# Kernel optimization log

Measured on AMD Instinct MI355X. Metric: run time of the kernel, lower is better.

The kernel has to match this reference:

```python
import jax, jax.numpy as jnp
import numpy as np
import math

B, S, D, H = 4, 1024, 1024, 16
F = 4 * D
DK = D // H

def layer_norm(x, g, b, eps=1e-5):
    mu = jnp.mean(x, axis=-1, keepdims=True)
    var = jnp.var(x, axis=-1, keepdims=True)
    return (x - mu) * jax.lax.rsqrt(var + eps) * g + b

def setup_inputs() -> dict:
    key = jax.random.key(0)
    ks = jax.random.split(key, 8)
    s = 0.02
    return {
        "x": jax.random.normal(ks[0], (B, S, D), dtype=jnp.float32),
        "Wq": jax.random.normal(ks[1], (D, D), dtype=jnp.float32) * s,
        "Wk": jax.random.normal(ks[2], (D, D), dtype=jnp.float32) * s,
        "Wv": jax.random.normal(ks[3], (D, D), dtype=jnp.float32) * s,
        "Wo": jax.random.normal(ks[4], (D, D), dtype=jnp.float32) * s,
        "w1": jax.random.normal(ks[5], (F, D), dtype=jnp.float32) * s,
        "b1": jnp.zeros((F,), dtype=jnp.float32),
        "w2": jax.random.normal(ks[6], (D, F), dtype=jnp.float32) * s,
        "b2": jnp.zeros((D,), dtype=jnp.float32),
        "ln1_g": jnp.ones((D,), dtype=jnp.float32),
        "ln1_b": jnp.zeros((D,), dtype=jnp.float32),
        "ln2_g": jnp.ones((D,), dtype=jnp.float32),
        "ln2_b": jnp.zeros((D,), dtype=jnp.float32),
        "mask": jnp.ones((B, S, S), dtype=jnp.int32),
    }

def reference(x, Wq, Wk, Wv, Wo, w1, b1, w2, b2, ln1_g, ln1_b, ln2_g, ln2_b, mask):
    # --- attention sublayer (pre-norm residual) ---
    h = layer_norm(x, ln1_g, ln1_b)
    def split_heads(t):  # [B,S,D] -> [B,H,S,DK]
        return t.reshape(B, S, H, DK).transpose(0, 2, 1, 3)
    q = split_heads(h @ Wq.T)
    k = split_heads(h @ Wk.T)
    v = split_heads(h @ Wv.T)
    scores = jnp.einsum('bhqd,bhkd->bhqk', q, k) / math.sqrt(DK)
    m = (mask[:, None, :, :] != 0)  # [B,1,S,S] broadcast over heads
    scores = jnp.where(m, scores, -1e9)
    p = jax.nn.softmax(scores, axis=-1)
    p = jnp.where(m, p, 0.0)
    ctx = jnp.einsum('bhqk,bhkd->bhqd', p, v)
    ctx = ctx.transpose(0, 2, 1, 3).reshape(B, S, D)
    x = x + ctx @ Wo.T
    # --- FFN sublayer (pre-norm residual) ---
    h2 = layer_norm(x, ln2_g, ln2_b)
    y = jax.nn.gelu(h2 @ w1.T + b1, approximate=False) @ w2.T + b2
    row_valid = jnp.sum(mask, axis=-1) > 0  # [B,S]
    y = jnp.where(row_valid[..., None], y, 0.0)
    return x + y
```

## Files before the change

kernel.cpp:

```cpp
#include <hip/hip_runtime.h>

typedef unsigned short u16;
typedef unsigned int   u32;
typedef unsigned long long u64;

typedef __bf16 bf16_t;
typedef bf16_t bf16x8 __attribute__((ext_vector_type(8)));
typedef float  f32x4  __attribute__((ext_vector_type(4)));

static constexpr int Bz = 4, Sq = 1024, Dm = 1024, Hn = 16, Ff = 4096, Mtok = 4096;
static constexpr int QS = 3072;

static __device__ __forceinline__ u16 f2bf(float f) {
  u32 u = __builtin_bit_cast(u32, f);
  u32 r = u + 0x7fff + ((u >> 16) & 1);
  return (u16)(r >> 16);
}

static __device__ __forceinline__ void gld16(const u16* g, u16* l) {
  __builtin_amdgcn_global_load_lds((const __attribute__((address_space(1))) u32*)g,
                                   (__attribute__((address_space(3))) u32*)l, 16, 0, 0);
}

__global__ void k_cvt(const float* __restrict__ src, u16* __restrict__ dst, int n4) {
  int i = blockIdx.x * 256 + threadIdx.x;
  if (i >= n4) return;
  float4 v = reinterpret_cast<const float4*>(src)[i];
  ushort4 o;
  o.x = f2bf(v.x); o.y = f2bf(v.y); o.z = f2bf(v.z); o.w = f2bf(v.w);
  reinterpret_cast<ushort4*>(dst)[i] = o;
}

__global__ void k_maskpack(const int* __restrict__ mask, u32* __restrict__ mb,
                           u32* __restrict__ rv) {
  int row = blockIdx.x;
  int t = threadIdx.x, w = t >> 6, lane = t & 63;
  const int* mrow = mask + (size_t)row * Sq;
  __shared__ u32 red[4];
  u32 any = 0;
#pragma unroll
  for (int i = 0; i < 4; i++) {
    int chunk = w * 4 + i;
    int k = chunk * 64 + lane;
    u64 bal = __ballot(mrow[k] != 0);
    any |= (u32)(bal | (bal >> 32));
    if (lane == 0) mb[(size_t)row * 32 + chunk * 2]     = (u32)bal;
    if (lane == 1) mb[(size_t)row * 32 + chunk * 2 + 1] = (u32)(bal >> 32);
  }
  if (lane == 0) red[w] = any;
  __syncthreads();
  if (t == 0) rv[row] = (red[0] | red[1] | red[2] | red[3]) ? 1u : 0u;
}

__global__ void k_ln(const float* __restrict__ x, const float* __restrict__ g,
                     const float* __restrict__ bb, u16* __restrict__ out) {
  int row = blockIdx.x, t = threadIdx.x;
  float4 v = reinterpret_cast<const float4*>(x + (size_t)row * Dm)[t];
  float s  = v.x + v.y + v.z + v.w;
  float s2 = v.x * v.x + v.y * v.y + v.z * v.z + v.w * v.w;
#pragma unroll
  for (int m = 1; m < 64; m <<= 1) { s += __shfl_xor(s, m); s2 += __shfl_xor(s2, m); }
  __shared__ float rs[4], rs2[4];
  int w = t >> 6;
  if ((t & 63) == 0) { rs[w] = s; rs2[w] = s2; }
  __syncthreads();
  s  = rs[0] + rs[1] + rs[2] + rs[3];
  s2 = rs2[0] + rs2[1] + rs2[2] + rs2[3];
  float mu  = s * (1.0f / Dm);
  float var = s2 * (1.0f / Dm) - mu * mu;
  float r = rsqrtf(var + 1e-5f);
  float4 gv = reinterpret_cast<const float4*>(g)[t];
  float4 bv = reinterpret_cast<const float4*>(bb)[t];
  ushort4 o;
  o.x = f2bf((v.x - mu) * r * gv.x + bv.x);
  o.y = f2bf((v.y - mu) * r * gv.y + bv.y);
  o.z = f2bf((v.z - mu) * r * gv.z + bv.z);
  o.w = f2bf((v.w - mu) * r * gv.w + bv.w);
  reinterpret_cast<ushort4*>(out + (size_t)row * Dm)[t] = o;
}

template <int MODE>
__global__ __launch_bounds__(256)
void k_gemm(const u16* __restrict__ A, const u16* __restrict__ Bw,
            int M, int N, int K,
            const float* __restrict__ bias, void* __restrict__ Cout) {
  __shared__ u16 As[128 * 64];
  __shared__ u16 Bs[128 * 64];
  const int t = threadIdx.x;
  const int lane = t & 63, w = t >> 6;
  const int wr = w >> 1, wc = w & 1;
  const int m0 = blockIdx.y * 128, n0 = blockIdx.x * 128;
  const int lr = lane & 15, lk = (lane >> 4) * 8;

  f32x4 acc[4][4] = {};

  for (int kt = 0; kt < K; kt += 64) {
#pragma unroll
    for (int i = 0; i < 4; i++) {
      int cc = i * 256 + t; int row = cc >> 3, c8 = cc & 7;
      gld16(A + (size_t)(m0 + row) * K + kt + c8 * 8, &As[cc * 8]);
    }
#pragma unroll
    for (int i = 0; i < 4; i++) {
      int cc = i * 256 + t; int row = cc >> 3, c8 = cc & 7;
      gld16(Bw + (size_t)(n0 + row) * K + kt + c8 * 8, &Bs[cc * 8]);
    }
    __syncthreads();
#pragma unroll
    for (int kk = 0; kk < 2; kk++) {
      bf16x8 af[4], bfg[4];
#pragma unroll
      for (int m = 0; m < 4; m++)
        af[m] = *reinterpret_cast<const bf16x8*>(&As[(wr * 64 + m * 16 + lr) * 64 + kk * 32 + lk]);
#pragma unroll
      for (int n = 0; n < 4; n++)
        bfg[n] = *reinterpret_cast<const bf16x8*>(&Bs[(wc * 64 + n * 16 + lr) * 64 + kk * 32 + lk]);
#pragma unroll
      for (int m = 0; m < 4; m++)
#pragma unroll
        for (int n = 0; n < 4; n++)
          acc[m][n] = __builtin_amdgcn_mfma_f32_16x16x32_bf16(af[m], bfg[n], acc[m][n], 0, 0, 0);
    }
    __syncthreads();
  }

#pragma unroll
  for (int m = 0; m < 4; m++) {
    const int rowb = m0 + wr * 64 + m * 16 + (lane >> 4) * 4;
#pragma unroll
    for (int n = 0; n < 4; n++) {
      const int col = n0 + wc * 64 + n * 16 + lr;
#pragma unroll
      for (int r = 0; r < 4; r++) {
        const int row = rowb + r;
        float v = acc[m][n][r];
        size_t idx = (size_t)row * N + col;
        if constexpr (MODE == 0) {
          ((u16*)Cout)[idx] = f2bf(v);
        } else {
          float xx = v + bias[col];
          float gl = 0.5f * xx * (1.0f + erff(xx * 0.70710678118f));
          ((u16*)Cout)[idx] = f2bf(gl);
        }
      }
    }
  }
}

template <int MODE>
__global__ __launch_bounds__(256)
void k_gemm64(const u16* __restrict__ A, const u16* __restrict__ Bw,
              int M, int N, int K,
              const float* __restrict__ resid, const float* __restrict__ bias,
              const u32* __restrict__ rv, float* __restrict__ Cout) {
  __shared__ u16 As[128 * 64];
  __shared__ u16 Bs[64 * 64];
  const int t = threadIdx.x;
  const int lane = t & 63, w = t >> 6;
  const int m0 = blockIdx.y * 128, n0 = blockIdx.x * 64;
  const int lr = lane & 15, lk = (lane >> 4) * 8;

  f32x4 acc[2][4] = {};

  for (int kt = 0; kt < K; kt += 64) {
#pragma unroll
    for (int i = 0; i < 4; i++) {
      int cc = i * 256 + t; int row = cc >> 3, c8 = cc & 7;
      gld16(A + (size_t)(m0 + row) * K + kt + c8 * 8, &As[cc * 8]);
    }
#pragma unroll
    for (int i = 0; i < 2; i++) {
      int cc = i * 256 + t; int row = cc >> 3, c8 = cc & 7;
      gld16(Bw + (size_t)(n0 + row) * K + kt + c8 * 8, &Bs[cc * 8]);
    }
    __syncthreads();
#pragma unroll
    for (int kk = 0; kk < 2; kk++) {
      bf16x8 af[2], bfg[4];
#pragma unroll
      for (int m = 0; m < 2; m++)
        af[m] = *reinterpret_cast<const bf16x8*>(&As[(w * 32 + m * 16 + lr) * 64 + kk * 32 + lk]);
#pragma unroll
      for (int n = 0; n < 4; n++)
        bfg[n] = *reinterpret_cast<const bf16x8*>(&Bs[(n * 16 + lr) * 64 + kk * 32 + lk]);
#pragma unroll
      for (int m = 0; m < 2; m++)
#pragma unroll
        for (int n = 0; n < 4; n++)
          acc[m][n] = __builtin_amdgcn_mfma_f32_16x16x32_bf16(af[m], bfg[n], acc[m][n], 0, 0, 0);
    }
    __syncthreads();
  }

#pragma unroll
  for (int m = 0; m < 2; m++) {
    const int rowb = m0 + w * 32 + m * 16 + (lane >> 4) * 4;
#pragma unroll
    for (int n = 0; n < 4; n++) {
      const int col = n0 + n * 16 + lr;
#pragma unroll
      for (int r = 0; r < 4; r++) {
        const int row = rowb + r;
        float v = acc[m][n][r];
        size_t idx = (size_t)row * N + col;
        if constexpr (MODE == 1) {
          Cout[idx] = resid[idx] + v;
        } else {
          float y = rv[row] ? (v + bias[col]) : 0.0f;
          Cout[idx] = resid[idx] + y;
        }
      }
    }
  }
}

__global__ __launch_bounds__(256)
void k_attn(const u16* __restrict__ qkv, const u32* __restrict__ mb,
            u16* __restrict__ ctxb) {
  __shared__ u16 Qs[64 * 64];
  __shared__ u16 Ks[64 * 64];
  __shared__ u16 Vts[64 * 64];
  __shared__ u16 Ps[4 * 16 * 64];
  const int t = threadIdx.x, lane = t & 63, w = t >> 6;
  const int q0 = blockIdx.x * 64;
  const int bh = blockIdx.y, b = bh >> 4, h = bh & 15;
  const int lr = lane & 15, lkq = (lane >> 4) * 8;
  const size_t baseq = (size_t)(b * Sq) * QS + h * 64;

  {
    int r = t >> 2, c0 = (t & 3) * 16;
    const u16* gp = qkv + baseq + (size_t)(q0 + r) * QS + c0;
    uint4 v0 = *reinterpret_cast<const uint4*>(gp);
    uint4 v1 = *reinterpret_cast<const uint4*>(gp + 8);
    int sw = (r & 7) << 3;
    *reinterpret_cast<uint4*>(&Qs[r * 64 + (c0 ^ sw)]) = v0;
    *reinterpret_cast<uint4*>(&Qs[r * 64 + ((c0 + 8) ^ sw)]) = v1;
  }
  __syncthreads();

  bf16x8 qf[2];
  const int qrow = w * 16 + lr;
#pragma unroll
  for (int kk = 0; kk < 2; kk++)
    qf[kk] = *reinterpret_cast<const bf16x8*>(&Qs[qrow * 64 + ((kk * 32 + lkq) ^ ((qrow & 7) << 3))]);

  float m_i[4] = {-1e30f, -1e30f, -1e30f, -1e30f};
  float l_i[4] = {0.f, 0.f, 0.f, 0.f};
  f32x4 accO[4] = {};
  const int rq0 = (lane >> 4) * 4;

  for (int kt = 0; kt < Sq / 64; kt++) {
    __syncthreads();
    {
      int r = t >> 2, c0 = (t & 3) * 16;
      const u16* gp = qkv + baseq + 1024 + (size_t)(kt * 64 + r) * QS + c0;
      uint4 v0 = *reinterpret_cast<const uint4*>(gp);
      uint4 v1 = *reinterpret_cast<const uint4*>(gp + 8);
      int sw = (r & 7) << 3;
      *reinterpret_cast<uint4*>(&Ks[r * 64 + (c0 ^ sw)]) = v0;
      *reinterpret_cast<uint4*>(&Ks[r * 64 + ((c0 + 8) ^ sw)]) = v1;
      const u16* gv = qkv + baseq + 2048 + (size_t)(kt * 64 + r) * QS + c0;
      u16 tmp[16];
      *reinterpret_cast<uint4*>(&tmp[0]) = *reinterpret_cast<const uint4*>(gv);
      *reinterpret_cast<uint4*>(&tmp[8]) = *reinterpret_cast<const uint4*>(gv + 8);
#pragma unroll
      for (int j = 0; j < 16; j++) {
        int d = c0 + j;
        Vts[d * 64 + (r ^ ((d & 7) << 3))] = tmp[j];
      }
    }
    __syncthreads();

    f32x4 sc[4];
#pragma unroll
    for (int n = 0; n < 4; n++) sc[n] = (f32x4){0.f, 0.f, 0.f, 0.f};
#pragma unroll
    for (int kk = 0; kk < 2; kk++) {
#pragma unroll
      for (int n = 0; n < 4; n++) {
        int krow = n * 16 + lr;
        bf16x8 kf = *reinterpret_cast<const bf16x8*>(
            &Ks[krow * 64 + ((kk * 32 + lkq) ^ ((krow & 7) << 3))]);
        sc[n] = __builtin_amdgcn_mfma_f32_16x16x32_bf16(qf[kk], kf, sc[n], 0, 0, 0);
      }
    }
    u32 mw[4][2];
#pragma unroll
    for (int r = 0; r < 4; r++) {
      int q = q0 + w * 16 + rq0 + r;
      mw[r][0] = mb[(size_t)(b * Sq + q) * 32 + kt * 2];
      mw[r][1] = mb[(size_t)(b * Sq + q) * 32 + kt * 2 + 1];
    }
    float rmax[4] = {-1e30f, -1e30f, -1e30f, -1e30f};
#pragma unroll
    for (int n = 0; n < 4; n++) {
      int kin = n * 16 + lr;
#pragma unroll
      for (int r = 0; r < 4; r++) {
        float sval = sc[n][r] * 0.125f;
        if (!((mw[r][kin >> 5] >> (kin & 31)) & 1)) sval = -1e9f;
        sc[n][r] = sval;
        rmax[r] = fmaxf(rmax[r], sval);
      }
    }
#pragma unroll
    for (int r = 0; r < 4; r++) {
#pragma unroll
      for (int mm = 1; mm < 16; mm <<= 1) rmax[r] = fmaxf(rmax[r], __shfl_xor(rmax[r], mm));
      float mnew = fmaxf(m_i[r], rmax[r]);
      float scale = __expf(m_i[r] - mnew);
      m_i[r] = mnew;
      l_i[r] *= scale;
#pragma unroll
      for (int n = 0; n < 4; n++) accO[n][r] *= scale;
    }
    float rsum[4] = {0.f, 0.f, 0.f, 0.f};
#pragma unroll
    for (int n = 0; n < 4; n++)
#pragma unroll
      for (int r = 0; r < 4; r++) {
        float p = __expf(sc[n][r] - m_i[r]);
        sc[n][r] = p;
        rsum[r] += p;
      }
#pragma unroll
    for (int r = 0; r < 4; r++) {
#pragma unroll
      for (int mm = 1; mm < 16; mm <<= 1) rsum[r] += __shfl_xor(rsum[r], mm);
      l_i[r] += rsum[r];
    }
#pragma unroll
    for (int n = 0; n < 4; n++)
#pragma unroll
      for (int r = 0; r < 4; r++) {
        int row = rq0 + r;
        Ps[w * 1024 + row * 64 + ((n * 16 + lr) ^ ((row & 7) << 3))] = f2bf(sc[n][r]);
      }
    asm volatile("s_waitcnt lgkmcnt(0)" ::: "memory");
    __builtin_amdgcn_sched_barrier(0);
    bf16x8 pf[2];
#pragma unroll
    for (int kk = 0; kk < 2; kk++)
      pf[kk] = *reinterpret_cast<const bf16x8*>(
          &Ps[w * 1024 + lr * 64 + ((kk * 32 + lkq) ^ ((lr & 7) << 3))]);
#pragma unroll
    for (int kk = 0; kk < 2; kk++) {
#pragma unroll
      for (int n = 0; n < 4; n++) {
        int d = n * 16 + lr;
        bf16x8 vf = *reinterpret_cast<const bf16x8*>(
            &Vts[d * 64 + ((kk * 32 + lkq) ^ ((d & 7) << 3))]);
        accO[n] = __builtin_amdgcn_mfma_f32_16x16x32_bf16(pf[kk], vf, accO[n], 0, 0, 0);
      }
    }
  }

#pragma unroll
  for (int r = 0; r < 4; r++) {
    float recip = (m_i[r] <= -0.9e9f || l_i[r] == 0.f) ? 0.f : 1.f / l_i[r];
    int grow = q0 + w * 16 + rq0 + r;
#pragma unroll
    for (int n = 0; n < 4; n++)
      ctxb[(size_t)(b * Sq + grow) * Dm + h * 64 + n * 16 + lr] = f2bf(accO[n][r] * recip);
  }
}

extern "C" void kernel_launch(void* const* d_in, const int* in_sizes, int n_in,
                              void* d_out, int out_size, void* d_ws, size_t ws_size,
                              hipStream_t stream) {
  const float* x     = (const float*)d_in[0];
  const float* Wq    = (const float*)d_in[1];
  const float* Wk    = (const float*)d_in[2];
  const float* Wv    = (const float*)d_in[3];
  const float* Wo    = (const float*)d_in[4];
  const float* w1    = (const float*)d_in[5];
  const float* b1    = (const float*)d_in[6];
  const float* w2    = (const float*)d_in[7];
  const float* b2    = (const float*)d_in[8];
  const float* ln1g  = (const float*)d_in[9];
  const float* ln1b  = (const float*)d_in[10];
  const float* ln2g  = (const float*)d_in[11];
  const float* ln2b  = (const float*)d_in[12];
  const int*   mask  = (const int*)d_in[13];
  float* out = (float*)d_out;

  char* ws = (char*)d_ws;
  const size_t MB = 1024 * 1024;
  u16* wqkv_b = (u16*)(ws + 0 * MB);
  u16* wo_b   = (u16*)(ws + 13 * MB / 2);
  u16* w1_b   = (u16*)(ws + 17 * MB / 2);
  u16* w2_b   = (u16*)(ws + 17 * MB);
  u16* h_b    = (u16*)(ws + 51 * MB / 2);
  u32* mbits  = (u32*)(ws + 34 * MB);
  u32* rv     = (u32*)(ws + 34 * MB + 600 * 1024);
  u16* qkv    = (u16*)(ws + 35 * MB);
  u16* ctxb   = (u16*)(ws + 121 * MB / 2);
  u16* a1b    = (u16*)(ws + 35 * MB);
  float* x1   = out;

  k_cvt<<<1024, 256, 0, stream>>>(Wq, wqkv_b,               262144);
  k_cvt<<<1024, 256, 0, stream>>>(Wk, wqkv_b + 1024 * 1024, 262144);
  k_cvt<<<1024, 256, 0, stream>>>(Wv, wqkv_b + 2048 * 1024, 262144);
  k_cvt<<<1024, 256, 0, stream>>>(Wo, wo_b, 262144);
  k_cvt<<<4096, 256, 0, stream>>>(w1, w1_b, 1048576);
  k_cvt<<<4096, 256, 0, stream>>>(w2, w2_b, 1048576);
  k_maskpack<<<4096, 256, 0, stream>>>(mask, mbits, rv);
  k_ln<<<4096, 256, 0, stream>>>(x, ln1g, ln1b, h_b);

  dim3 gqkv(QS / 128, Mtok / 128);
  k_gemm<0><<<gqkv, 256, 0, stream>>>(h_b, wqkv_b, Mtok, QS, Dm, nullptr, qkv);

  dim3 ga(Sq / 64, Bz * Hn);
  k_attn<<<ga, 256, 0, stream>>>(qkv, mbits, ctxb);

  dim3 gwo(Dm / 64, Mtok / 128);
  k_gemm64<1><<<gwo, 256, 0, stream>>>(ctxb, wo_b, Mtok, Dm, Dm, x, nullptr, nullptr, x1);

  k_ln<<<4096, 256, 0, stream>>>(x1, ln2g, ln2b, h_b);

  dim3 g2(Ff / 128, Mtok / 128);
  k_gemm<2><<<g2, 256, 0, stream>>>(h_b, w1_b, Mtok, Ff, Dm, b1, a1b);

  dim3 gw2(Dm / 64, Mtok / 128);
  k_gemm64<3><<<gw2, 256, 0, stream>>>(a1b, w2_b, Mtok, Dm, Ff, x1, b2, rv, out);
}
```

Measured before the change: 456.4 us.

## Emit transposed V from QKV GEMM and double-buffer K/V loads in attention

The QKV GEMM now writes the V slice directly in a per-head transposed layout, so attention no longer transposes V element by element through LDS. Attention stages K and V tiles with async global-to-LDS loads into double buffers and prefetches the next tile while computing the current one. It also adds a fast path for fully unmasked mask words and skips the softmax rescale unless the running max grows by more than 8. The lazy rescale keeps exponents bounded relative to a stale max, which trades a small range risk for fewer exp and multiply operations.

```diff
diff --git a/kernel.cpp b/kernel.cpp
--- a/kernel.cpp
+++ b/kernel.cpp
@@ -83,7 +83,8 @@
 __global__ __launch_bounds__(256)
 void k_gemm(const u16* __restrict__ A, const u16* __restrict__ Bw,
             int M, int N, int K,
-            const float* __restrict__ bias, void* __restrict__ Cout) {
+            const float* __restrict__ bias, void* __restrict__ Cout,
+            u16* __restrict__ vTout) {
   __shared__ u16 As[128 * 64];
   __shared__ u16 Bs[128 * 64];
   const int t = threadIdx.x;
@@ -122,6 +123,26 @@
           acc[m][n] = __builtin_amdgcn_mfma_f32_16x16x32_bf16(af[m], bfg[n], acc[m][n], 0, 0, 0);
     }
     __syncthreads();
+  }
+
+  if constexpr (MODE == 0) {
+    if (n0 >= 2048) {
+#pragma unroll
+      for (int m = 0; m < 4; m++) {
+        const int rowb = m0 + wr * 64 + m * 16 + (lane >> 4) * 4;
+        const int bb = rowb >> 10, tok = rowb & 1023;
+#pragma unroll
+        for (int n = 0; n < 4; n++) {
+          const int dfull = n0 + wc * 64 + n * 16 + lr - 2048;
+          ushort4 o4;
+          o4.x = f2bf(acc[m][n][0]); o4.y = f2bf(acc[m][n][1]);
+          o4.z = f2bf(acc[m][n][2]); o4.w = f2bf(acc[m][n][3]);
+          size_t idx = ((size_t)((bb * 16 + (dfull >> 6)) * 64 + (dfull & 63))) * 1024 + tok;
+          *reinterpret_cast<ushort4*>(vTout + idx) = o4;
+        }
+      }
+      return;
+    }
   }
 
 #pragma unroll
@@ -215,27 +236,46 @@
 }
 
 __global__ __launch_bounds__(256)
-void k_attn(const u16* __restrict__ qkv, const u32* __restrict__ mb,
-            u16* __restrict__ ctxb) {
-  __shared__ u16 Qs[64 * 64];
-  __shared__ u16 Ks[64 * 64];
-  __shared__ u16 Vts[64 * 64];
-  __shared__ u16 Ps[4 * 16 * 64];
+void k_attn(const u16* __restrict__ qkv, const u16* __restrict__ vT,
+            const u32* __restrict__ mb, u16* __restrict__ ctxb) {
+  __shared__ u16 Qs[4096];
+  __shared__ u16 Ks0[4096];
+  __shared__ u16 Vt0[4096];
+  __shared__ u16 Vt1[4096];
+  __shared__ u16 Ps[4096];
   const int t = threadIdx.x, lane = t & 63, w = t >> 6;
   const int q0 = blockIdx.x * 64;
   const int bh = blockIdx.y, b = bh >> 4, h = bh & 15;
   const int lr = lane & 15, lkq = (lane >> 4) * 8;
-  const size_t baseq = (size_t)(b * Sq) * QS + h * 64;
+
+  const size_t qbase = (size_t)(b * Sq + q0) * QS + h * 64;
+  const size_t kbase = (size_t)(b * Sq) * QS + 1024 + h * 64;
+  const size_t vbase = (size_t)bh * 64 * 1024;
+
+  auto stageK = [&](u16* dst, int kt) {
+#pragma unroll
+    for (int j = 0; j < 2; j++) {
+      int cc = j * 256 + t, r = cc >> 3, ch = cc & 7;
+      gld16(qkv + kbase + (size_t)(kt * 64 + r) * QS + ((ch ^ (r & 7)) * 8), dst + cc * 8);
+    }
+  };
+  auto stageV = [&](u16* dst, int kt) {
+#pragma unroll
+    for (int j = 0; j < 2; j++) {
+      int cc = j * 256 + t, d = cc >> 3, ch = cc & 7;
+      gld16(vT + vbase + (size_t)d * 1024 + kt * 64 + ((ch ^ (d & 7)) * 8), dst + cc * 8);
+    }
+  };
 
   {
-    int r = t >> 2, c0 = (t & 3) * 16;
-    const u16* gp = qkv + baseq + (size_t)(q0 + r) * QS + c0;
-    uint4 v0 = *reinterpret_cast<const uint4*>(gp);
-    uint4 v1 = *reinterpret_cast<const uint4*>(gp + 8);
-    int sw = (r & 7) << 3;
-    *reinterpret_cast<uint4*>(&Qs[r * 64 + (c0 ^ sw)]) = v0;
-    *reinterpret_cast<uint4*>(&Qs[r * 64 + ((c0 + 8) ^ sw)]) = v1;
-  }
+#pragma unroll
+    for (int j = 0; j < 2; j++) {
+      int cc = j * 256 + t, r = cc >> 3, ch = cc & 7;
+      gld16(qkv + qbase + (size_t)r * QS + ((ch ^ (r & 7)) * 8), &Qs[cc * 8]);
+    }
+  }
+  stageK(Ks0, 0);
+  stageV(Vt0, 0);
   __syncthreads();
 
   bf16x8 qf[2];
@@ -243,6 +283,7 @@
 #pragma unroll
   for (int kk = 0; kk < 2; kk++)
     qf[kk] = *reinterpret_cast<const bf16x8*>(&Qs[qrow * 64 + ((kk * 32 + lkq) ^ ((qrow & 7) << 3))]);
+  __syncthreads();
 
   float m_i[4] = {-1e30f, -1e30f, -1e30f, -1e30f};
   float l_i[4] = {0.f, 0.f, 0.f, 0.f};
@@ -250,26 +291,19 @@
   const int rq0 = (lane >> 4) * 4;
 
   for (int kt = 0; kt < Sq / 64; kt++) {
-    __syncthreads();
-    {
-      int r = t >> 2, c0 = (t & 3) * 16;
-      const u16* gp = qkv + baseq + 1024 + (size_t)(kt * 64 + r) * QS + c0;
-      uint4 v0 = *reinterpret_cast<const uint4*>(gp);
-      uint4 v1 = *reinterpret_cast<const uint4*>(gp + 8);
-      int sw = (r & 7) << 3;
-      *reinterpret_cast<uint4*>(&Ks[r * 64 + (c0 ^ sw)]) = v0;
-      *reinterpret_cast<uint4*>(&Ks[r * 64 + ((c0 + 8) ^ sw)]) = v1;
-      const u16* gv = qkv + baseq + 2048 + (size_t)(kt * 64 + r) * QS + c0;
-      u16 tmp[16];
-      *reinterpret_cast<uint4*>(&tmp[0]) = *reinterpret_cast<const uint4*>(gv);
-      *reinterpret_cast<uint4*>(&tmp[8]) = *reinterpret_cast<const uint4*>(gv + 8);
-#pragma unroll
-      for (int j = 0; j < 16; j++) {
-        int d = c0 + j;
-        Vts[d * 64 + (r ^ ((d & 7) << 3))] = tmp[j];
-      }
-    }
-    __syncthreads();
+    u16* kb = (kt & 1) ? Qs : Ks0;
+    u16* vb = (kt & 1) ? Vt1 : Vt0;
+    if (kt + 1 < Sq / 64) {
+      stageK((kt & 1) ? Ks0 : Qs, kt + 1);
+      stageV((kt & 1) ? Vt0 : Vt1, kt + 1);
+    }
+    u32 mw0[4], mw1[4];
+#pragma unroll
+    for (int r = 0; r < 4; r++) {
+      int q = q0 + w * 16 + rq0 + r;
+      mw0[r] = mb[(size_t)(b * Sq + q) * 32 + kt * 2];
+      mw1[r] = mb[(size_t)(b * Sq + q) * 32 + kt * 2 + 1];
+    }
 
     f32x4 sc[4];
 #pragma unroll
@@ -280,27 +314,31 @@
       for (int n = 0; n < 4; n++) {
         int krow = n * 16 + lr;
         bf16x8 kf = *reinterpret_cast<const bf16x8*>(
-            &Ks[krow * 64 + ((kk * 32 + lkq) ^ ((krow & 7) << 3))]);
+            &kb[krow * 64 + ((kk * 32 + lkq) ^ ((krow & 7) << 3))]);
         sc[n] = __builtin_amdgcn_mfma_f32_16x16x32_bf16(qf[kk], kf, sc[n], 0, 0, 0);
       }
     }
-    u32 mw[4][2];
+
+    float rmax[4] = {-1e30f, -1e30f, -1e30f, -1e30f};
 #pragma unroll
     for (int r = 0; r < 4; r++) {
-      int q = q0 + w * 16 + rq0 + r;
-      mw[r][0] = mb[(size_t)(b * Sq + q) * 32 + kt * 2];
-      mw[r][1] = mb[(size_t)(b * Sq + q) * 32 + kt * 2 + 1];
-    }
-    float rmax[4] = {-1e30f, -1e30f, -1e30f, -1e30f};
-#pragma unroll
-    for (int n = 0; n < 4; n++) {
-      int kin = n * 16 + lr;
-#pragma unroll
-      for (int r = 0; r < 4; r++) {
-        float sval = sc[n][r] * 0.125f;
-        if (!((mw[r][kin >> 5] >> (kin & 31)) & 1)) sval = -1e9f;
-        sc[n][r] = sval;
-        rmax[r] = fmaxf(rmax[r], sval);
+      if ((mw0[r] & mw1[r]) == 0xffffffffu) {
+#pragma unroll
+        for (int n = 0; n < 4; n++) {
+          float sval = sc[n][r] * 0.125f;
+          sc[n][r] = sval;
+          rmax[r] = fmaxf(rmax[r], sval);
+        }
+      } else {
+#pragma unroll
+        for (int n = 0; n < 4; n++) {
+          int kin = n * 16 + lr;
+          float sval = sc[n][r] * 0.125f;
+          u32 word = (kin & 32) ? mw1[r] : mw0[r];
+          if (!((word >> (kin & 31)) & 1)) sval = -1e9f;
+          sc[n][r] = sval;
+          rmax[r] = fmaxf(rmax[r], sval);
+        }
       }
     }
 #pragma unroll
@@ -308,11 +346,13 @@
 #pragma unroll
       for (int mm = 1; mm < 16; mm <<= 1) rmax[r] = fmaxf(rmax[r], __shfl_xor(rmax[r], mm));
       float mnew = fmaxf(m_i[r], rmax[r]);
-      float scale = __expf(m_i[r] - mnew);
-      m_i[r] = mnew;
-      l_i[r] *= scale;
-#pragma unroll
-      for (int n = 0; n < 4; n++) accO[n][r] *= scale;
+      if (mnew - m_i[r] > 8.0f) {
+        float scale = __expf(m_i[r] - mnew);
+        m_i[r] = mnew;
+        l_i[r] *= scale;
+#pragma unroll
+        for (int n = 0; n < 4; n++) accO[n][r] *= scale;
+      }
     }
     float rsum[4] = {0.f, 0.f, 0.f, 0.f};
 #pragma unroll
@@ -349,10 +389,11 @@
       for (int n = 0; n < 4; n++) {
         int d = n * 16 + lr;
         bf16x8 vf = *reinterpret_cast<const bf16x8*>(
-            &Vts[d * 64 + ((kk * 32 + lkq) ^ ((d & 7) << 3))]);
+            &vb[d * 64 + ((kk * 32 + lkq) ^ ((d & 7) << 3))]);
         accO[n] = __builtin_amdgcn_mfma_f32_16x16x32_bf16(pf[kk], vf, accO[n], 0, 0, 0);
       }
     }
+    __syncthreads();
   }
 
 #pragma unroll
@@ -395,6 +436,7 @@
   u32* rv     = (u32*)(ws + 34 * MB + 600 * 1024);
   u16* qkv    = (u16*)(ws + 35 * MB);
   u16* ctxb   = (u16*)(ws + 121 * MB / 2);
+  u16* vTb    = (u16*)(ws + 69 * MB);
   u16* a1b    = (u16*)(ws + 35 * MB);
   float* x1   = out;
 
@@ -408,10 +450,10 @@
   k_ln<<<4096, 256, 0, stream>>>(x, ln1g, ln1b, h_b);
 
   dim3 gqkv(QS / 128, Mtok / 128);
-  k_gemm<0><<<gqkv, 256, 0, stream>>>(h_b, wqkv_b, Mtok, QS, Dm, nullptr, qkv);
+  k_gemm<0><<<gqkv, 256, 0, stream>>>(h_b, wqkv_b, Mtok, QS, Dm, nullptr, qkv, vTb);
 
   dim3 ga(Sq / 64, Bz * Hn);
-  k_attn<<<ga, 256, 0, stream>>>(qkv, mbits, ctxb);
+  k_attn<<<ga, 256, 0, stream>>>(qkv, vTb, mbits, ctxb);
 
   dim3 gwo(Dm / 64, Mtok / 128);
   k_gemm64<1><<<gwo, 256, 0, stream>>>(ctxb, wo_b, Mtok, Dm, Dm, x, nullptr, nullptr, x1);
@@ -419,7 +461,7 @@
   k_ln<<<4096, 256, 0, stream>>>(x1, ln2g, ln2b, h_b);
 
   dim3 g2(Ff / 128, Mtok / 128);
-  k_gemm<2><<<g2, 256, 0, stream>>>(h_b, w1_b, Mtok, Ff, Dm, b1, a1b);
+  k_gemm<2><<<g2, 256, 0, stream>>>(h_b, w1_b, Mtok, Ff, Dm, b1, a1b, nullptr);
 
   dim3 gw2(Dm / 64, Mtok / 128);
   k_gemm64<3><<<gw2, 256, 0, stream>>>(a1b, w2_b, Mtok, Dm, Ff, x1, b2, rv, out);
```

Result: no change. 454.1 us (-0.5%).
